# Optimization experiments

Hardware: AMD Instinct MI355X
Metric: run time of the kernel (lower is better)

The kernel has to match this reference:

```python
import jax, jax.numpy as jnp
import numpy as np

B, T, D, H, L, K, DFF = 8, 512, 512, 8, 4, 31, 2048
DK = D // H
PAD = (K - 1) // 2

def _ln(x, g, b, eps=1e-5):
    m = x.mean(-1, keepdims=True)
    v = ((x - m) ** 2).mean(-1, keepdims=True)
    return (x - m) * jax.lax.rsqrt(v + eps) * g + b

def _swish(x):
    return x * jax.nn.sigmoid(x)

def _rel_shift(x):
    # x: [B,H,T,P] with P = 2T-1 (Transformer-XL style shift)
    b, h, q, p = x.shape
    x = jnp.pad(x, ((0, 0), (0, 0), (0, 0), (1, 0)))
    x = x.reshape(b, h, p + 1, q)[:, :, 1:].reshape(b, h, q, p)
    return x

def setup_inputs() -> dict:
    key = jax.random.key(0)
    ks = iter(jax.random.split(key, 64))
    def w(shape, s=0.02):
        return jax.random.normal(next(ks), shape, jnp.float32) * s
    inp = {
        'x': jax.random.normal(next(ks), (B, T, D), jnp.float32),
        'pos_emb': jax.random.normal(next(ks), (1, 2 * T - 1, D), jnp.float32),
        'ln1_g': jnp.ones((L, D)), 'ln1_b': jnp.zeros((L, D)),
        'ff1_w1': w((L, D, DFF)), 'ff1_b1': jnp.zeros((L, DFF)),
        'ff1_w2': w((L, DFF, D)), 'ff1_b2': jnp.zeros((L, D)),
        'lnA_g': jnp.ones((L, D)), 'lnA_b': jnp.zeros((L, D)),
        'Wq': w((L, D, D)), 'bq': jnp.zeros((L, D)),
        'Wk': w((L, D, D)), 'bk': jnp.zeros((L, D)),
        'Wv': w((L, D, D)), 'bv': jnp.zeros((L, D)),
        'Wo': w((L, D, D)), 'bo': jnp.zeros((L, D)),
        'Wpos': w((L, D, D)),
        'pbu': jnp.zeros((L, H, DK)), 'pbv': jnp.zeros((L, H, DK)),
        'lnC_g': jnp.ones((L, D)), 'lnC_b': jnp.zeros((L, D)),
        'pw1_w': w((L, 2 * D, D)), 'pw1_b': jnp.zeros((L, 2 * D)),
        'dw_w': w((L, D, K)), 'dw_b': jnp.zeros((L, D)),
        'cln_g': jnp.ones((L, D)), 'cln_b': jnp.zeros((L, D)),
        'pw2_w': w((L, D, D)), 'pw2_b': jnp.zeros((L, D)),
        'ln2_g': jnp.ones((L, D)), 'ln2_b': jnp.zeros((L, D)),
        'ff2_w1': w((L, D, DFF)), 'ff2_b1': jnp.zeros((L, DFF)),
        'ff2_w2': w((L, DFF, D)), 'ff2_b2': jnp.zeros((L, D)),
        'lnO_g': jnp.ones((L, D)), 'lnO_b': jnp.zeros((L, D)),
    }
    return inp

def reference(x, pos_emb, ln1_g, ln1_b, ff1_w1, ff1_b1, ff1_w2, ff1_b2,
              lnA_g, lnA_b, Wq, bq, Wk, bk, Wv, bv, Wo, bo, Wpos, pbu, pbv,
              lnC_g, lnC_b, pw1_w, pw1_b, dw_w, dw_b, cln_g, cln_b, pw2_w, pw2_b,
              ln2_g, ln2_b, ff2_w1, ff2_b1, ff2_w2, ff2_b2, lnO_g, lnO_b):
    scale = 1.0 / np.sqrt(DK).astype(np.float32)
    for i in range(L):
        # FFN 1 (half-step residual)
        res = x
        y = _ln(x, ln1_g[i], ln1_b[i])
        y = _swish(y @ ff1_w1[i] + ff1_b1[i]) @ ff1_w2[i] + ff1_b2[i]
        res = res + 0.5 * y
        # rel-pos multi-head self-attention
        y = _ln(res, lnA_g[i], lnA_b[i])
        q = (y @ Wq[i] + bq[i]).reshape(B, T, H, DK)
        k = (y @ Wk[i] + bk[i]).reshape(B, T, H, DK)
        v = (y @ Wv[i] + bv[i]).reshape(B, T, H, DK)
        p = (pos_emb @ Wpos[i]).reshape(1, 2 * T - 1, H, DK)
        ac = jnp.einsum('bthd,bshd->bhts', q + pbu[i], k)          # content score
        bd = jnp.einsum('bthd,xshd->bhts', q + pbv[i], p)          # position score
        bd = _rel_shift(bd)[..., :T]
        attn = jax.nn.softmax((ac + bd) * scale, axis=-1)
        o = jnp.einsum('bhts,bshd->bthd', attn, v).reshape(B, T, D)
        res = res + (o @ Wo[i] + bo[i])
        # convolution module
        y = _ln(res, lnC_g[i], lnC_b[i])
        y = y @ pw1_w[i].T + pw1_b[i]                               # (B,T,2D)
        a, g = jnp.split(y, 2, axis=-1)
        y = a * jax.nn.sigmoid(g)                                   # GLU over channels
        y = jax.lax.conv_general_dilated(
            y.transpose(0, 2, 1), dw_w[i][:, None, :],
            window_strides=(1,), padding=[(PAD, PAD)],
            feature_group_count=D,
            dimension_numbers=('NCH', 'OIH', 'NCH'))
        y = y.transpose(0, 2, 1) + dw_b[i]                          # (B,T,D)
        y = _swish(_ln(y, cln_g[i], cln_b[i]))
        y = y @ pw2_w[i].T + pw2_b[i]
        res = res + y
        # FFN 2 (half-step residual)
        y = _ln(res, ln2_g[i], ln2_b[i])
        y = _swish(y @ ff2_w1[i] + ff2_b1[i]) @ ff2_w2[i] + ff2_b2[i]
        res = res + 0.5 * y
        x = _ln(res, lnO_g[i], lnO_b[i])
    return x
```

## Files before the change

kernel.cpp:

```cpp
#include <hip/hip_runtime.h>


typedef unsigned short u16;
typedef unsigned int u32;
typedef __attribute__((ext_vector_type(8))) short bf16x8;
typedef __attribute__((ext_vector_type(4))) float f32x4;

#define DI __device__ __forceinline__

constexpr int CT = 512;
constexpr int CD = 512;
constexpr int CH = 8;
constexpr int CDK = 64;
constexpr int CDFF = 2048;
constexpr int CNBT = 4096;
constexpr int CL = 4;

DI u16 f2bf(float f) {
  u32 u = __builtin_bit_cast(u32, f);
  u = u + 0x7fffu + ((u >> 16) & 1u);
  return (u16)(u >> 16);
}
DI float bf2f(u16 h) { u32 u = ((u32)h) << 16; return __builtin_bit_cast(float, u); }
DI u32 pack2(float a, float b) { return (u32)f2bf(a) | ((u32)f2bf(b) << 16); }
DI float sigm(float x) { return 1.0f / (1.0f + __expf(-x)); }

DI f32x4 MFMA(bf16x8 a, bf16x8 b, f32x4 c) {
  return __builtin_amdgcn_mfma_f32_16x16x32_bf16(a, b, c, 0, 0, 0);
}

DI void gload16(const void* g, void* l) {
  __builtin_amdgcn_global_load_lds((const __attribute__((address_space(1))) void*)g,
                                   (__attribute__((address_space(3))) void*)l, 16, 0, 0);
}

DI float wsum(float v) {
#pragma unroll
  for (int o = 32; o > 0; o >>= 1) v += __shfl_xor(v, o, 64);
  return v;
}

DI void tbody(const float* ip, u16* op, int R, int C, int c0, int r0,
              int tx, int ty) {
  __shared__ float t[32][33];
#pragma unroll
  for (int i = ty; i < 32; i += 8)
    t[i][tx] = ip[(long)(r0 + i) * C + c0 + tx];
  __syncthreads();
#pragma unroll
  for (int i = ty; i < 32; i += 8)
    op[(long)(c0 + i) * R + r0 + tx] = f2bf(t[tx][i]);
}

__global__ __launch_bounds__(256) void tconv2x_k(const float* __restrict__ in0,
                                                 const float* __restrict__ in1,
                                                 u16* __restrict__ out0,
                                                 u16* __restrict__ out1,
                                                 int R, int C) {
  int z = blockIdx.z;
  int l = z & 3;
  const float* ip = (z < 4 ? in0 : in1) + (long)l * R * C;
  u16* op = (z < 4 ? out0 : out1) + (long)l * R * C;
  tbody(ip, op, R, C, blockIdx.x * 32, blockIdx.y * 32, threadIdx.x, threadIdx.y);
}

__global__ __launch_bounds__(256) void tconvQ_k(
    const float* __restrict__ Wq, const float* __restrict__ Wk,
    const float* __restrict__ Wv, const float* __restrict__ Wo,
    const float* __restrict__ Wpos, u16* __restrict__ wt_qkv,
    u16* __restrict__ wt_o, u16* __restrict__ wt_pos) {
  int z = blockIdx.z;
  int sel = z >> 2, l = z & 3;
  const float* ip;
  u16* op;
  const long S = 512L * 512;
  switch (sel) {
    case 0: ip = Wq + l * S; op = wt_qkv + (long)l * 1536 * 512; break;
    case 1: ip = Wk + l * S; op = wt_qkv + (long)l * 1536 * 512 + S; break;
    case 2: ip = Wv + l * S; op = wt_qkv + (long)l * 1536 * 512 + 2 * S; break;
    case 3: ip = Wo + l * S; op = wt_o + l * S; break;
    default: ip = Wpos + l * S; op = wt_pos + l * S; break;
  }
  tbody(ip, op, 512, 512, blockIdx.x * 32, blockIdx.y * 32, threadIdx.x, threadIdx.y);
}

__global__ __launch_bounds__(256) void cvt_k(const float* __restrict__ in,
                                             u16* __restrict__ out, long nIn, long nOut,
                                             long inZ, long outZ) {
  long i = ((long)blockIdx.x * 256 + threadIdx.x) * 4;
  if (i >= nOut) return;
  const float* ip = in + (long)blockIdx.y * inZ;
  u16* op = out + (long)blockIdx.y * outZ;
  u16 o[4];
#pragma unroll
  for (int j = 0; j < 4; ++j) {
    long idx = i + j;
    o[j] = (idx < nIn) ? f2bf(ip[idx]) : (u16)0;
  }
  uint2 st;
  st.x = (u32)o[0] | ((u32)o[1] << 16);
  st.y = (u32)o[2] | ((u32)o[3] << 16);
  *(uint2*)&op[i] = st;
}

__global__ __launch_bounds__(256) void pwperm_k(const float* __restrict__ in,
                                                u16* __restrict__ out) {
  int l = blockIdx.y;
  long i = (long)blockIdx.x * 256 + threadIdx.x;
  long n = i >> 7;
  int c = (int)(i & 127) * 4;
  int q = (int)(n >> 4) & 1;
  long r = (q ? 512 : 0) + ((n >> 5) << 4) + (n & 15);
  const float* ip = in + ((long)l * 1024 + r) * 512 + c;
  float4 v = *(const float4*)ip;
  u16* op = out + ((long)l * 1024 + n) * 512 + c;
  uint2 st;
  st.x = pack2(v.x, v.y);
  st.y = pack2(v.z, v.w);
  *(uint2*)op = st;
}

__global__ __launch_bounds__(256) void dwt_k(const float* __restrict__ in,
                                             float* __restrict__ out) {
  int l = blockIdx.y;
  int idx = blockIdx.x * 256 + threadIdx.x;
  if (idx >= 512 * 31) return;
  int k = idx >> 9, d = idx & 511;
  out[(long)l * 31 * 512 + idx] = in[(long)l * 512 * 31 + d * 31 + k];
}

__global__ __launch_bounds__(256) void qkvbias_k(const float* __restrict__ bq,
                                                 const float* __restrict__ bk,
                                                 const float* __restrict__ bv,
                                                 float* __restrict__ out) {
  int z = blockIdx.y;
  int j = blockIdx.x * 256 + threadIdx.x;
  float v;
  if (j < 512) v = bq[z * 512 + j];
  else if (j < 1024) v = bk[z * 512 + j - 512];
  else v = bv[z * 512 + j - 1024];
  out[z * 1536 + j] = v;
}

__global__ __launch_bounds__(256) void copy_k(const float* __restrict__ in,
                                              float* __restrict__ out) {
  long i = ((long)blockIdx.x * 256 + threadIdx.x) * 4;
  *(float4*)(out + i) = *(const float4*)(in + i);
}

template <int F32OUT>
__global__ __launch_bounds__(256) void ln_k(const float* in, void* out,
                                            const float* gw, const float* bw) {
  int tid = threadIdx.x, wid = tid >> 6, lane = tid & 63;
  long row = (long)blockIdx.x * 4 + wid;
  const float* x = in + row * CD + lane * 8;
  float4 v0 = *(const float4*)x;
  float4 v1 = *(const float4*)(x + 4);
  float s = v0.x + v0.y + v0.z + v0.w + v1.x + v1.y + v1.z + v1.w;
  float q = v0.x * v0.x + v0.y * v0.y + v0.z * v0.z + v0.w * v0.w +
            v1.x * v1.x + v1.y * v1.y + v1.z * v1.z + v1.w * v1.w;
  s = wsum(s);
  q = wsum(q);
  float mean = s * (1.0f / CD);
  float var = q * (1.0f / CD) - mean * mean;
  float rs = rsqrtf(var + 1e-5f);
  int c = lane * 8;
  float4 g0 = *(const float4*)(gw + c), g1 = *(const float4*)(gw + c + 4);
  float4 b0 = *(const float4*)(bw + c), b1 = *(const float4*)(bw + c + 4);
  float y0 = (v0.x - mean) * rs * g0.x + b0.x;
  float y1 = (v0.y - mean) * rs * g0.y + b0.y;
  float y2 = (v0.z - mean) * rs * g0.z + b0.z;
  float y3 = (v0.w - mean) * rs * g0.w + b0.w;
  float y4 = (v1.x - mean) * rs * g1.x + b1.x;
  float y5 = (v1.y - mean) * rs * g1.y + b1.y;
  float y6 = (v1.z - mean) * rs * g1.z + b1.z;
  float y7 = (v1.w - mean) * rs * g1.w + b1.w;
  if (F32OUT) {
    float* o = (float*)out + row * CD + c;
    *(float4*)o = make_float4(y0, y1, y2, y3);
    *(float4*)(o + 4) = make_float4(y4, y5, y6, y7);
  } else {
    u16* o = (u16*)out + row * CD + c;
    uint4 pk;
    pk.x = pack2(y0, y1);
    pk.y = pack2(y2, y3);
    pk.z = pack2(y4, y5);
    pk.w = pack2(y6, y7);
    *(uint4*)o = pk;
  }
}

__global__ __launch_bounds__(256) void lnln_k(float* cur, u16* ybf,
                                              const float* gO, const float* bO,
                                              const float* g1, const float* b1) {
  int tid = threadIdx.x, wid = tid >> 6, lane = tid & 63;
  long row = (long)blockIdx.x * 4 + wid;
  float* x = cur + row * CD + lane * 8;
  float v[8];
  *(float4*)&v[0] = *(const float4*)x;
  *(float4*)&v[4] = *(const float4*)(x + 4);
  float s = 0.f, q = 0.f;
#pragma unroll
  for (int j = 0; j < 8; ++j) { s += v[j]; q += v[j] * v[j]; }
  s = wsum(s);
  q = wsum(q);
  float mean = s * (1.0f / CD);
  float var = q * (1.0f / CD) - mean * mean;
  float rs = rsqrtf(var + 1e-5f);
  int c = lane * 8;
  float y[8];
#pragma unroll
  for (int j = 0; j < 8; ++j) y[j] = (v[j] - mean) * rs * gO[c + j] + bO[c + j];
  *(float4*)x = *(float4*)&y[0];
  *(float4*)(x + 4) = *(float4*)&y[4];
  float s2 = 0.f, q2 = 0.f;
#pragma unroll
  for (int j = 0; j < 8; ++j) { s2 += y[j]; q2 += y[j] * y[j]; }
  s2 = wsum(s2);
  q2 = wsum(q2);
  float mean2 = s2 * (1.0f / CD);
  float var2 = q2 * (1.0f / CD) - mean2 * mean2;
  float rs2 = rsqrtf(var2 + 1e-5f);
  float z[8];
#pragma unroll
  for (int j = 0; j < 8; ++j) z[j] = (y[j] - mean2) * rs2 * g1[c + j] + b1[c + j];
  u16* o = ybf + row * CD + c;
  uint4 pk;
  pk.x = pack2(z[0], z[1]);
  pk.y = pack2(z[2], z[3]);
  pk.z = pack2(z[4], z[5]);
  pk.w = pack2(z[6], z[7]);
  *(uint4*)o = pk;
}

template <int EPI, int SPLITK>
__global__ __launch_bounds__(256, 3) void gemm3_k(
    const u16* __restrict__ A, const u16* __restrict__ B, void* C,
    const float* __restrict__ bias, float alpha, int lda, int ldb, int ldc, int Kd) {
  __shared__ u16 ldsA[2][128 * 64];
  __shared__ u16 ldsB[2][64 * 64];
  const int tid = threadIdx.x, wid = tid >> 6, lane = tid & 63;
  const int m0 = blockIdx.x * 128, n0 = blockIdx.y * 64;
  const int wm = wid >> 1, wn = wid & 1;
  const int fr = lane & 15, fq = lane >> 4;
  const f32x4 vz = {0.f, 0.f, 0.f, 0.f};
  f32x4 acc[4][2] = {{vz, vz}, {vz, vz}, {vz, vz}, {vz, vz}};

  const int Kc = Kd / SPLITK;
  const int kb0 = (SPLITK > 1) ? blockIdx.z * Kc : 0;
  const int nK = Kc / 64;

  auto stage = [&](int buf, int kt) {
    const int k0 = kb0 + kt * 64;
#pragma unroll
    for (int r = 0; r < 4; ++r) {
      int bi = r * 4096 + tid * 16;
      int row = bi >> 7;
      int ch = ((bi >> 4) & 7) ^ (row & 7);
      gload16(A + (long)(m0 + row) * lda + k0 + ch * 8,
              (char*)&ldsA[buf][0] + r * 4096 + wid * 1024);
    }
#pragma unroll
    for (int r = 0; r < 2; ++r) {
      int bi = r * 4096 + tid * 16;
      int row = bi >> 7;
      int ch = ((bi >> 4) & 7) ^ (row & 7);
      gload16(B + (long)(n0 + row) * ldb + k0 + ch * 8,
              (char*)&ldsB[buf][0] + r * 4096 + wid * 1024);
    }
  };

  stage(0, 0);
  asm volatile("s_waitcnt vmcnt(0)" ::: "memory");
  __syncthreads();
  int buf = 0;
  for (int kt = 0; kt < nK; ++kt) {
    if (kt + 1 < nK) stage(buf ^ 1, kt + 1);
#pragma unroll
    for (int ks = 0; ks < 2; ++ks) {
      int ch = ks * 4 + fq;
      bf16x8 af[4], bfv[2];
#pragma unroll
      for (int i = 0; i < 4; ++i) {
        int arow = wm * 64 + i * 16 + fr;
        af[i] = *(const bf16x8*)((const char*)&ldsA[buf][0] + arow * 128 +
                                 ((ch ^ (arow & 7)) << 4));
      }
#pragma unroll
      for (int i = 0; i < 2; ++i) {
        int brow = wn * 32 + i * 16 + fr;
        bfv[i] = *(const bf16x8*)((const char*)&ldsB[buf][0] + brow * 128 +
                                  ((ch ^ (brow & 7)) << 4));
      }
#pragma unroll
      for (int mi = 0; mi < 4; ++mi)
#pragma unroll
        for (int ni = 0; ni < 2; ++ni)
          acc[mi][ni] = MFMA(af[mi], bfv[ni], acc[mi][ni]);
    }
    asm volatile("s_waitcnt vmcnt(0)" ::: "memory");
    __syncthreads();
    buf ^= 1;
  }

  if constexpr (EPI == 7) {
    const int ucol = (n0 >> 1) + wn * 16 + fr;
    float ba = bias[ucol], bg = bias[512 + ucol];
#pragma unroll
    for (int mi = 0; mi < 4; ++mi) {
      const int gmB = m0 + wm * 64 + mi * 16 + fq * 4;
#pragma unroll
      for (int r = 0; r < 4; ++r) {
        float va = acc[mi][0][r] + ba;
        float vg = acc[mi][1][r] + bg;
        ((u16*)C)[(long)(gmB + r) * 512 + ucol] = f2bf(va * sigm(vg));
      }
    }
  } else {
#pragma unroll
    for (int mi = 0; mi < 4; ++mi) {
      const int gmB = m0 + wm * 64 + mi * 16 + fq * 4;
#pragma unroll
      for (int ni = 0; ni < 2; ++ni) {
        const int gn = n0 + wn * 32 + ni * 16 + fr;
        float bv_ = 0.f;
        if constexpr (EPI == 1 || EPI == 2 || EPI == 3) bv_ = bias[gn];
#pragma unroll
        for (int r = 0; r < 4; ++r) {
          const int gm = gmB + r;
          float v = acc[mi][ni][r];
          long idx = (long)gm * ldc + gn;
          if constexpr (EPI == 0) ((u16*)C)[idx] = f2bf(v);
          else if constexpr (EPI == 1) ((u16*)C)[idx] = f2bf(v + bv_);
          else if constexpr (EPI == 2) {
            float x = v + bv_;
            ((u16*)C)[idx] = f2bf(x * sigm(x));
          } else if constexpr (EPI == 3) {
            float* R = (float*)C;
            if constexpr (SPLITK > 1) {
              float add = alpha * (v + (blockIdx.z == 0 ? bv_ : 0.f));
              atomicAdd(&R[idx], add);
            } else {
              R[idx] += alpha * (v + bv_);
            }
          }
        }
      }
    }
  }
}

__global__ __launch_bounds__(256) void vtrans_k(const u16* __restrict__ qkv,
                                                u16* __restrict__ vt) {
  __shared__ u16 t[64][80];
  int tid = threadIdx.x;
  int t0 = blockIdx.x * 64;
  int bh = blockIdx.y, b = bh >> 3, h = bh & 7;
  {
    int tl = tid >> 2, dg = (tid & 3) * 16;
    const u16* src = qkv + ((long)(b * CT + t0 + tl)) * 1536 + 1024 + h * 64 + dg;
    uint4 a0 = *(const uint4*)src;
    uint4 a1 = *(const uint4*)(src + 8);
    *(uint4*)&t[tl][dg] = a0;
    *(uint4*)&t[tl][dg + 8] = a1;
  }
  __syncthreads();
  {
    int dl = tid >> 2, tg = (tid & 3) * 16;
    u16* dst = vt + ((long)bh * 64 + dl) * CT + t0 + tg;
    u16 tmp[16];
#pragma unroll
    for (int j = 0; j < 16; ++j) tmp[j] = t[tg + j][dl];
    uint4 o0, o1;
    o0.x = (u32)tmp[0] | ((u32)tmp[1] << 16);
    o0.y = (u32)tmp[2] | ((u32)tmp[3] << 16);
    o0.z = (u32)tmp[4] | ((u32)tmp[5] << 16);
    o0.w = (u32)tmp[6] | ((u32)tmp[7] << 16);
    o1.x = (u32)tmp[8] | ((u32)tmp[9] << 16);
    o1.y = (u32)tmp[10] | ((u32)tmp[11] << 16);
    o1.z = (u32)tmp[12] | ((u32)tmp[13] << 16);
    o1.w = (u32)tmp[14] | ((u32)tmp[15] << 16);
    *(uint4*)dst = o0;
    *(uint4*)(dst + 8) = o1;
  }
}

__global__ __launch_bounds__(256, 2) void attn_k(
    const u16* __restrict__ qkvp, const u16* __restrict__ pball,
    const float* __restrict__ pbuL, const float* __restrict__ pbvL,
    const u16* __restrict__ vt, u16* __restrict__ out) {
  __shared__ u16 ldsK[2][64 * 64];
  __shared__ u16 ldsP[2][128 * 64];
  __shared__ u16 bd0s[4][16 * 80];
  __shared__ u16 stile[4][16 * 64];
  const int tid = threadIdx.x, wid = tid >> 6, lane = tid & 63;
  const int t0 = blockIdx.x * 64;
  const int bh = blockIdx.y, b = bh >> 3, h = bh & 7;
  const int fr = lane & 15, fq = lane >> 4;

  const u16* kbase = qkvp + (long)(b * CT) * 1536 + 512 + h * 64;
  const u16* pbase = pball + h * 64;
  const float* pu = pbuL + h * 64;
  const float* pv = pbvL + h * 64;

  const u16* qp = qkvp + (long)(b * CT + t0 + wid * 16 + fr) * 1536 + h * 64;
  bf16x8 qua[2], qva[2];
#pragma unroll
  for (int kk = 0; kk < 2; ++kk) {
    bf16x8 qw = *(const bf16x8*)(qp + kk * 32 + fq * 8);
    const float* bu = pu + kk * 32 + fq * 8;
    const float* bv = pv + kk * 32 + fq * 8;
#pragma unroll
    for (int j = 0; j < 8; ++j) {
      float qf = bf2f((u16)qw[j]);
      qua[kk][j] = (short)f2bf(qf + bu[j]);
      qva[kk][j] = (short)f2bf(qf + bv[j]);
    }
  }

  const f32x4 vz = {0.f, 0.f, 0.f, 0.f};
  f32x4 oacc[4] = {vz, vz, vz, vz};
  float m_run[4] = {-1e30f, -1e30f, -1e30f, -1e30f};
  float l_run[4] = {0.f, 0.f, 0.f, 0.f};
  const int jbw = (3 - wid) * 16;

  auto stage = [&](int buf, int st) {
    int s0 = st * 64, j0 = s0 - t0 + 448;
#pragma unroll
    for (int r = 0; r < 2; ++r) {
      int c = r * 256 + tid;
      int row = c >> 3, cs = (c & 7) ^ (row & 7);
      gload16(kbase + (long)(s0 + row) * 1536 + cs * 8,
              (char*)&ldsK[buf][0] + r * 4096 + wid * 1024);
    }
#pragma unroll
    for (int r = 0; r < 4; ++r) {
      int c = r * 256 + tid;
      int row = c >> 3, cs = (c & 7) ^ (row & 7);
      gload16(pbase + (long)(j0 + row) * 2048 + cs * 8,
              (char*)&ldsP[buf][0] + r * 4096 + wid * 1024);
    }
  };

  stage(0, 0);
  int cur = 0;
  for (int st = 0; st < 8; ++st) {
    const int s0 = st * 64;
    if (st + 1 < 8) {
      stage(cur ^ 1, st + 1);
      asm volatile("s_waitcnt vmcnt(6)" ::: "memory");
    } else {
      asm volatile("s_waitcnt vmcnt(0)" ::: "memory");
    }
    __syncthreads();

    bf16x8 vb[4][2];
#pragma unroll
    for (int ni = 0; ni < 4; ++ni)
#pragma unroll
      for (int kk = 0; kk < 2; ++kk)
        vb[ni][kk] = *(const bf16x8*)&vt[((long)bh * 64 + ni * 16 + fr) * 512 +
                                         s0 + kk * 32 + fq * 8];

    f32x4 ac[4] = {vz, vz, vz, vz};
#pragma unroll
    for (int kk = 0; kk < 2; ++kk) {
#pragma unroll
      for (int ni = 0; ni < 4; ++ni) {
        int row = ni * 16 + fr;
        bf16x8 kb = *(const bf16x8*)((const char*)&ldsK[cur][0] +
                                     ((row * 128 + kk * 64 + fq * 16) ^ ((row & 7) << 4)));
        ac[ni] = MFMA(qua[kk], kb, ac[ni]);
      }
    }
    f32x4 bd[5] = {vz, vz, vz, vz, vz};
#pragma unroll
    for (int kk = 0; kk < 2; ++kk) {
#pragma unroll
      for (int nbi = 0; nbi < 5; ++nbi) {
        int row = jbw + nbi * 16 + fr;
        bf16x8 pb = *(const bf16x8*)((const char*)&ldsP[cur][0] +
                                     ((row * 128 + kk * 64 + fq * 16) ^ ((row & 7) << 4)));
        bd[nbi] = MFMA(qva[kk], pb, bd[nbi]);
      }
    }
#pragma unroll
    for (int nbi = 0; nbi < 5; ++nbi)
#pragma unroll
      for (int r = 0; r < 4; ++r)
        bd0s[wid][(fq * 4 + r) * 80 + nbi * 16 + fr] = f2bf(bd[nbi][r]);

    float vals[4][4];
#pragma unroll
    for (int ni = 0; ni < 4; ++ni)
#pragma unroll
      for (int r = 0; r < 4; ++r) {
        int tlw = fq * 4 + r;
        int jcol = ni * 16 + fr + 15 - tlw;
        vals[ni][r] = (ac[ni][r] + bf2f(bd0s[wid][tlw * 80 + jcol])) * 0.125f;
      }
    float scf[4];
#pragma unroll
    for (int r = 0; r < 4; ++r) {
      float mx = fmaxf(fmaxf(vals[0][r], vals[1][r]), fmaxf(vals[2][r], vals[3][r]));
      mx = fmaxf(mx, __shfl_xor(mx, 1));
      mx = fmaxf(mx, __shfl_xor(mx, 2));
      mx = fmaxf(mx, __shfl_xor(mx, 4));
      mx = fmaxf(mx, __shfl_xor(mx, 8));
      float mnew = fmaxf(m_run[r], mx);
      scf[r] = __expf(m_run[r] - mnew);
      m_run[r] = mnew;
      float sum = 0.f;
#pragma unroll
      for (int ni = 0; ni < 4; ++ni) {
        float p = __expf(vals[ni][r] - mnew);
        vals[ni][r] = p;
        sum += p;
      }
      sum += __shfl_xor(sum, 1);
      sum += __shfl_xor(sum, 2);
      sum += __shfl_xor(sum, 4);
      sum += __shfl_xor(sum, 8);
      l_run[r] = l_run[r] * scf[r] + sum;
    }
#pragma unroll
    for (int ni = 0; ni < 4; ++ni)
#pragma unroll
      for (int r = 0; r < 4; ++r) {
        int tlw = fq * 4 + r;
        *(u16*)((char*)&stile[wid][0] +
                (((tlw * 128) + (ni * 16 + fr) * 2) ^ ((tlw & 7) << 4))) =
            f2bf(vals[ni][r]);
      }
#pragma unroll
    for (int ni = 0; ni < 4; ++ni)
#pragma unroll
      for (int r = 0; r < 4; ++r) oacc[ni][r] *= scf[r];
#pragma unroll
    for (int kk = 0; kk < 2; ++kk) {
      bf16x8 pa = *(const bf16x8*)((const char*)&stile[wid][0] +
                                   ((fr * 128 + kk * 64 + fq * 16) ^ ((fr & 7) << 4)));
#pragma unroll
      for (int ni = 0; ni < 4; ++ni) oacc[ni] = MFMA(pa, vb[ni][kk], oacc[ni]);
    }
    __syncthreads();
    cur ^= 1;
  }

  float inv[4];
#pragma unroll
  for (int r = 0; r < 4; ++r) inv[r] = 1.0f / l_run[r];
#pragma unroll
  for (int ni = 0; ni < 4; ++ni)
#pragma unroll
    for (int r = 0; r < 4; ++r) {
      long row = (long)(b * CT + t0 + wid * 16 + fq * 4 + r) * CD + h * CDK;
      out[row + ni * 16 + fr] = f2bf(oacc[ni][r] * inv[r]);
    }
}

__global__ __launch_bounds__(256) void conv2_k(const u16* __restrict__ u,
                                               const float* __restrict__ wT,
                                               const float* __restrict__ wb,
                                               const float* __restrict__ cg,
                                               const float* __restrict__ cb,
                                               u16* __restrict__ out) {
  constexpr int TT = 8;
  int tid = threadIdx.x, d0 = tid * 2;
  int b = blockIdx.y, t0 = blockIdx.x * TT;
  const u16* ub = u + ((long)b * CT) * CD + d0;

  u32 strip[TT + 30];
#pragma unroll
  for (int j = 0; j < TT + 30; ++j) {
    int tt = t0 + j - 15;
    strip[j] = ((unsigned)tt < (unsigned)CT) ? *(const u32*)(ub + (long)tt * CD) : 0u;
  }
  float2 bias = *(const float2*)(wb + d0);
  float a0[TT], a1[TT];
#pragma unroll
  for (int t = 0; t < TT; ++t) { a0[t] = bias.x; a1[t] = bias.y; }
#pragma unroll
  for (int k = 0; k < 31; ++k) {
    float2 wk = *(const float2*)(wT + k * CD + d0);
#pragma unroll
    for (int t = 0; t < TT; ++t) {
      u32 pr = strip[t + k];
      a0[t] += bf2f((u16)(pr & 0xffff)) * wk.x;
      a1[t] += bf2f((u16)(pr >> 16)) * wk.y;
    }
  }
  __shared__ float redS[4][TT], redQ[4][TT];
  int wid = tid >> 6, lane = tid & 63;
#pragma unroll
  for (int t = 0; t < TT; ++t) {
    float s = a0[t] + a1[t];
    float q = a0[t] * a0[t] + a1[t] * a1[t];
    s = wsum(s);
    q = wsum(q);
    if (lane == 0) { redS[wid][t] = s; redQ[wid][t] = q; }
  }
  __syncthreads();
  float2 g2 = *(const float2*)(cg + d0);
  float2 b2 = *(const float2*)(cb + d0);
#pragma unroll
  for (int t = 0; t < TT; ++t) {
    float s = redS[0][t] + redS[1][t] + redS[2][t] + redS[3][t];
    float q = redQ[0][t] + redQ[1][t] + redQ[2][t] + redQ[3][t];
    float mean = s * (1.f / 512), var = q * (1.f / 512) - mean * mean;
    float rs = rsqrtf(var + 1e-5f);
    float y0 = (a0[t] - mean) * rs * g2.x + b2.x;
    float y1 = (a1[t] - mean) * rs * g2.y + b2.y;
    y0 = y0 * sigm(y0);
    y1 = y1 * sigm(y1);
    *(u32*)(out + ((long)(b * CT + t0 + t)) * CD + d0) = pack2(y0, y1);
  }
}

extern "C" void kernel_launch(void* const* d_in, const int* in_sizes, int n_in,
                              void* d_out, int out_size, void* d_ws, size_t ws_size,
                              hipStream_t stream) {
  const float* in_x   = (const float*)d_in[0];
  const float* in_pos = (const float*)d_in[1];
  const float* ln1_g  = (const float*)d_in[2];
  const float* ln1_b  = (const float*)d_in[3];
  const float* ff1_w1 = (const float*)d_in[4];
  const float* ff1_b1 = (const float*)d_in[5];
  const float* ff1_w2 = (const float*)d_in[6];
  const float* ff1_b2 = (const float*)d_in[7];
  const float* lnA_g  = (const float*)d_in[8];
  const float* lnA_b  = (const float*)d_in[9];
  const float* Wq     = (const float*)d_in[10];
  const float* bq     = (const float*)d_in[11];
  const float* Wk     = (const float*)d_in[12];
  const float* bk     = (const float*)d_in[13];
  const float* Wv     = (const float*)d_in[14];
  const float* bv     = (const float*)d_in[15];
  const float* Wo     = (const float*)d_in[16];
  const float* bo     = (const float*)d_in[17];
  const float* Wpos   = (const float*)d_in[18];
  const float* pbu    = (const float*)d_in[19];
  const float* pbv    = (const float*)d_in[20];
  const float* lnC_g  = (const float*)d_in[21];
  const float* lnC_b  = (const float*)d_in[22];
  const float* pw1_w  = (const float*)d_in[23];
  const float* pw1_b  = (const float*)d_in[24];
  const float* dw_w   = (const float*)d_in[25];
  const float* dw_b   = (const float*)d_in[26];
  const float* cln_g  = (const float*)d_in[27];
  const float* cln_b  = (const float*)d_in[28];
  const float* pw2_w  = (const float*)d_in[29];
  const float* pw2_b  = (const float*)d_in[30];
  const float* ln2_g  = (const float*)d_in[31];
  const float* ln2_b  = (const float*)d_in[32];
  const float* ff2_w1 = (const float*)d_in[33];
  const float* ff2_b1 = (const float*)d_in[34];
  const float* ff2_w2 = (const float*)d_in[35];
  const float* ff2_b2 = (const float*)d_in[36];
  const float* lnO_g  = (const float*)d_in[37];
  const float* lnO_b  = (const float*)d_in[38];
  (void)in_sizes; (void)n_in; (void)out_size; (void)ws_size;

  char* ws = (char*)d_ws;
  size_t off = 0;
  auto alloc = [&](size_t bytes) -> void* {
    off = (off + 255) & ~(size_t)255;
    void* p = ws + off;
    off += bytes;
    return p;
  };

  u16* wt_ff1w1 = (u16*)alloc((size_t)CL * CDFF * CD * 2);
  u16* wt_ff1w2 = (u16*)alloc((size_t)CL * CD * CDFF * 2);
  u16* wt_qkv   = (u16*)alloc((size_t)CL * 1536 * CD * 2);
  u16* wt_o     = (u16*)alloc((size_t)CL * CD * CD * 2);
  u16* wt_pos   = (u16*)alloc((size_t)CL * CD * CD * 2);
  u16* w_pw1p   = (u16*)alloc((size_t)CL * 1024 * CD * 2);
  u16* w_pw2    = (u16*)alloc((size_t)CL * CD * CD * 2);
  u16* wt_ff2w1 = (u16*)alloc((size_t)CL * CDFF * CD * 2);
  u16* wt_ff2w2 = (u16*)alloc((size_t)CL * CD * CDFF * 2);
  float* qkvbias = (float*)alloc((size_t)CL * 1536 * 4);
  u16* posbf = (u16*)alloc((size_t)1024 * CD * 2);
  float* dwT = (float*)alloc((size_t)CL * 31 * CD * 4);
  u16* pbf_all = (u16*)alloc((size_t)1024 * 2048 * 2);
  float* cur = (float*)alloc((size_t)CNBT * CD * 4);
  u16* ybf   = (u16*)alloc((size_t)CNBT * CD * 2);
  u16* qkv   = (u16*)alloc((size_t)CNBT * 1536 * 2);
  u16* hbf   = (u16*)alloc((size_t)CNBT * CDFF * 2);
  u16* vt    = (u16*)alloc((size_t)64 * CDK * CT * 2);
  u16* obf   = (u16*)alloc((size_t)CNBT * CD * 2);
  u16* ubuf  = (u16*)alloc((size_t)CNBT * CD * 2);
  u16* cbf   = (u16*)alloc((size_t)CNBT * CD * 2);

  dim3 b256(256);
  dim3 tb(32, 8);

  tconv2x_k<<<dim3(CDFF / 32, CD / 32, 2 * CL), tb, 0, stream>>>(
      ff1_w1, ff2_w1, wt_ff1w1, wt_ff2w1, CD, CDFF);
  tconv2x_k<<<dim3(CD / 32, CDFF / 32, 2 * CL), tb, 0, stream>>>(
      ff1_w2, ff2_w2, wt_ff1w2, wt_ff2w2, CDFF, CD);
  tconvQ_k<<<dim3(CD / 32, CD / 32, 5 * CL), tb, 0, stream>>>(
      Wq, Wk, Wv, Wo, Wpos, wt_qkv, wt_o, wt_pos);
  pwperm_k<<<dim3(512, CL), b256, 0, stream>>>(pw1_w, w_pw1p);
  cvt_k<<<dim3(256, CL, 1), b256, 0, stream>>>(pw2_w, w_pw2, 512L * 512, 512L * 512,
                                               512L * 512, 512L * 512);
  cvt_k<<<dim3(512, 1, 1), b256, 0, stream>>>(in_pos, posbf, 1023L * 512, 1024L * 512, 0, 0);
  dwt_k<<<dim3(62, CL), b256, 0, stream>>>(dw_w, dwT);
  qkvbias_k<<<dim3(6, CL), b256, 0, stream>>>(bq, bk, bv, qkvbias);
  copy_k<<<dim3(2048), b256, 0, stream>>>(in_x, cur);
  gemm3_k<0, 1><<<dim3(8, 32, 1), b256, 0, stream>>>(
      posbf, wt_pos, pbf_all, nullptr, 0.f, CD, CD, 2048, CD);
  ln_k<0><<<dim3(1024), b256, 0, stream>>>(cur, ybf, ln1_g, ln1_b);

  for (int i = 0; i < CL; ++i) {
    const u16* Wf1 = wt_ff1w1 + (long)i * CDFF * CD;
    const u16* Wf2 = wt_ff1w2 + (long)i * CD * CDFF;
    const u16* Wqk = wt_qkv + (long)i * 1536 * CD;
    const u16* Wou = wt_o + (long)i * CD * CD;
    const u16* Wp1 = w_pw1p + (long)i * 1024 * CD;
    const u16* Wp2 = w_pw2 + (long)i * CD * CD;
    const u16* Wf3 = wt_ff2w1 + (long)i * CDFF * CD;
    const u16* Wf4 = wt_ff2w2 + (long)i * CD * CDFF;

    gemm3_k<2, 1><<<dim3(32, 32, 1), b256, 0, stream>>>(
        ybf, Wf1, hbf, ff1_b1 + (long)i * CDFF, 0.f, CD, CD, CDFF, CD);
    gemm3_k<3, 2><<<dim3(32, 8, 2), b256, 0, stream>>>(
        hbf, Wf2, cur, ff1_b2 + i * CD, 0.5f, CDFF, CDFF, CD, CDFF);

    ln_k<0><<<dim3(1024), b256, 0, stream>>>(cur, ybf, lnA_g + i * CD, lnA_b + i * CD);
    gemm3_k<1, 1><<<dim3(32, 24, 1), b256, 0, stream>>>(
        ybf, Wqk, qkv, qkvbias + i * 1536, 0.f, CD, CD, 1536, CD);
    vtrans_k<<<dim3(8, 64), b256, 0, stream>>>(qkv, vt);
    attn_k<<<dim3(8, 64), b256, 0, stream>>>(qkv, pbf_all + i * 512, pbu + i * 512,
                                             pbv + i * 512, vt, obf);
    gemm3_k<3, 2><<<dim3(32, 8, 2), b256, 0, stream>>>(
        obf, Wou, cur, bo + i * CD, 1.0f, CD, CD, CD, CD);

    ln_k<0><<<dim3(1024), b256, 0, stream>>>(cur, ybf, lnC_g + i * CD, lnC_b + i * CD);
    gemm3_k<7, 1><<<dim3(32, 16, 1), b256, 0, stream>>>(
        ybf, Wp1, ubuf, pw1_b + (long)i * 1024, 0.f, CD, CD, 512, CD);
    conv2_k<<<dim3(CT / 8, 8), b256, 0, stream>>>(ubuf, dwT + (long)i * 31 * CD,
                                                  dw_b + i * CD, cln_g + i * CD,
                                                  cln_b + i * CD, cbf);
    gemm3_k<3, 2><<<dim3(32, 8, 2), b256, 0, stream>>>(
        cbf, Wp2, cur, pw2_b + i * CD, 1.0f, CD, CD, CD, CD);

    ln_k<0><<<dim3(1024), b256, 0, stream>>>(cur, ybf, ln2_g + i * CD, ln2_b + i * CD);
    gemm3_k<2, 1><<<dim3(32, 32, 1), b256, 0, stream>>>(
        ybf, Wf3, hbf, ff2_b1 + (long)i * CDFF, 0.f, CD, CD, CDFF, CD);
    gemm3_k<3, 2><<<dim3(32, 8, 2), b256, 0, stream>>>(
        hbf, Wf4, cur, ff2_b2 + i * CD, 0.5f, CDFF, CDFF, CD, CDFF);

    if (i < CL - 1)
      lnln_k<<<dim3(1024), b256, 0, stream>>>(cur, ybf, lnO_g + i * CD, lnO_b + i * CD,
                                              ln1_g + (i + 1) * CD, ln1_b + (i + 1) * CD);
    else
      ln_k<1><<<dim3(1024), b256, 0, stream>>>(cur, d_out, lnO_g + i * CD, lnO_b + i * CD);
  }
}
```

Before: 892.9 us.

## Shrink GEMM tiles to 64x64 and fuse V transpose into QKV epilogue

The GEMM kernel moves from 128x64 to 64x64 output tiles with a shared LDS array, doubling grid sizes to fill more compute units on the 4096-row problems. Both K-substeps of fragments are loaded before the MFMAs are issued. A new epilogue writes the V slice of the QKV projection directly in transposed per-head layout, which removes the separate vtrans kernel launch and its round trip through memory. The Wo and pw2 projections drop split-K atomics in favour of plain accumulation. Smaller tiles lower data reuse per block and raise total global and LDS traffic, and the transposed V stores are narrow 8-byte scattered writes.

Measured after the change: 794.8 us. 11.0% less time.

```diff
diff --git a/kernel.cpp b/kernel.cpp
--- a/kernel.cpp
+++ b/kernel.cpp
@@ -234,17 +234,17 @@
 }
 
 template <int EPI, int SPLITK>
-__global__ __launch_bounds__(256, 3) void gemm3_k(
+__global__ __launch_bounds__(256, 2) void gemm2_k(
     const u16* __restrict__ A, const u16* __restrict__ B, void* C,
+    u16* __restrict__ Caux,
     const float* __restrict__ bias, float alpha, int lda, int ldb, int ldc, int Kd) {
-  __shared__ u16 ldsA[2][128 * 64];
-  __shared__ u16 ldsB[2][64 * 64];
+  __shared__ u16 lds[2][2][64 * 64];
   const int tid = threadIdx.x, wid = tid >> 6, lane = tid & 63;
-  const int m0 = blockIdx.x * 128, n0 = blockIdx.y * 64;
+  const int m0 = blockIdx.x * 64, n0 = blockIdx.y * 64;
   const int wm = wid >> 1, wn = wid & 1;
   const int fr = lane & 15, fq = lane >> 4;
   const f32x4 vz = {0.f, 0.f, 0.f, 0.f};
-  f32x4 acc[4][2] = {{vz, vz}, {vz, vz}, {vz, vz}, {vz, vz}};
+  f32x4 acc[2][2] = {{vz, vz}, {vz, vz}};
 
   const int Kc = Kd / SPLITK;
   const int kb0 = (SPLITK > 1) ? blockIdx.z * Kc : 0;
@@ -253,20 +253,14 @@
   auto stage = [&](int buf, int kt) {
     const int k0 = kb0 + kt * 64;
 #pragma unroll
-    for (int r = 0; r < 4; ++r) {
+    for (int r = 0; r < 2; ++r) {
       int bi = r * 4096 + tid * 16;
       int row = bi >> 7;
       int ch = ((bi >> 4) & 7) ^ (row & 7);
       gload16(A + (long)(m0 + row) * lda + k0 + ch * 8,
-              (char*)&ldsA[buf][0] + r * 4096 + wid * 1024);
-    }
-#pragma unroll
-    for (int r = 0; r < 2; ++r) {
-      int bi = r * 4096 + tid * 16;
-      int row = bi >> 7;
-      int ch = ((bi >> 4) & 7) ^ (row & 7);
+              (char*)&lds[buf][0][0] + r * 4096 + wid * 1024);
       gload16(B + (long)(n0 + row) * ldb + k0 + ch * 8,
-              (char*)&ldsB[buf][0] + r * 4096 + wid * 1024);
+              (char*)&lds[buf][1][0] + r * 4096 + wid * 1024);
     }
   };
 
@@ -276,28 +270,27 @@
   int buf = 0;
   for (int kt = 0; kt < nK; ++kt) {
     if (kt + 1 < nK) stage(buf ^ 1, kt + 1);
+    bf16x8 af[2][2], bfv[2][2];
 #pragma unroll
     for (int ks = 0; ks < 2; ++ks) {
       int ch = ks * 4 + fq;
-      bf16x8 af[4], bfv[2];
-#pragma unroll
-      for (int i = 0; i < 4; ++i) {
-        int arow = wm * 64 + i * 16 + fr;
-        af[i] = *(const bf16x8*)((const char*)&ldsA[buf][0] + arow * 128 +
-                                 ((ch ^ (arow & 7)) << 4));
-      }
 #pragma unroll
       for (int i = 0; i < 2; ++i) {
+        int arow = wm * 32 + i * 16 + fr;
+        af[ks][i] = *(const bf16x8*)((const char*)&lds[buf][0][0] + arow * 128 +
+                                     ((ch ^ (arow & 7)) << 4));
         int brow = wn * 32 + i * 16 + fr;
-        bfv[i] = *(const bf16x8*)((const char*)&ldsB[buf][0] + brow * 128 +
-                                  ((ch ^ (brow & 7)) << 4));
-      }
-#pragma unroll
-      for (int mi = 0; mi < 4; ++mi)
+        bfv[ks][i] = *(const bf16x8*)((const char*)&lds[buf][1][0] + brow * 128 +
+                                      ((ch ^ (brow & 7)) << 4));
+      }
+    }
+#pragma unroll
+    for (int ks = 0; ks < 2; ++ks)
+#pragma unroll
+      for (int mi = 0; mi < 2; ++mi)
 #pragma unroll
         for (int ni = 0; ni < 2; ++ni)
-          acc[mi][ni] = MFMA(af[mi], bfv[ni], acc[mi][ni]);
-    }
+          acc[mi][ni] = MFMA(af[ks][mi], bfv[ks][ni], acc[mi][ni]);
     asm volatile("s_waitcnt vmcnt(0)" ::: "memory");
     __syncthreads();
     buf ^= 1;
@@ -307,8 +300,8 @@
     const int ucol = (n0 >> 1) + wn * 16 + fr;
     float ba = bias[ucol], bg = bias[512 + ucol];
 #pragma unroll
-    for (int mi = 0; mi < 4; ++mi) {
-      const int gmB = m0 + wm * 64 + mi * 16 + fq * 4;
+    for (int mi = 0; mi < 2; ++mi) {
+      const int gmB = m0 + wm * 32 + mi * 16 + fq * 4;
 #pragma unroll
       for (int r = 0; r < 4; ++r) {
         float va = acc[mi][0][r] + ba;
@@ -316,10 +309,41 @@
         ((u16*)C)[(long)(gmB + r) * 512 + ucol] = f2bf(va * sigm(vg));
       }
     }
+  } else if constexpr (EPI == 8) {
+    if (n0 < 1024) {
+#pragma unroll
+      for (int mi = 0; mi < 2; ++mi) {
+        const int gmB = m0 + wm * 32 + mi * 16 + fq * 4;
+#pragma unroll
+        for (int ni = 0; ni < 2; ++ni) {
+          const int gn = n0 + wn * 32 + ni * 16 + fr;
+          float bv_ = bias[gn];
+#pragma unroll
+          for (int r = 0; r < 4; ++r)
+            ((u16*)C)[(long)(gmB + r) * ldc + gn] = f2bf(acc[mi][ni][r] + bv_);
+        }
+      }
+    } else {
+#pragma unroll
+      for (int mi = 0; mi < 2; ++mi) {
+        const int gmB = m0 + wm * 32 + mi * 16 + fq * 4;
+        const int b = gmB >> 9, t = gmB & 511;
+#pragma unroll
+        for (int ni = 0; ni < 2; ++ni) {
+          const int gn = n0 + wn * 32 + ni * 16 + fr;
+          const int h = (gn - 1024) >> 6, d = (gn - 1024) & 63;
+          float bv_ = bias[gn];
+          uint2 pk;
+          pk.x = pack2(acc[mi][ni][0] + bv_, acc[mi][ni][1] + bv_);
+          pk.y = pack2(acc[mi][ni][2] + bv_, acc[mi][ni][3] + bv_);
+          *(uint2*)&Caux[((long)(b * 8 + h) * 64 + d) * 512 + t] = pk;
+        }
+      }
+    }
   } else {
 #pragma unroll
-    for (int mi = 0; mi < 4; ++mi) {
-      const int gmB = m0 + wm * 64 + mi * 16 + fq * 4;
+    for (int mi = 0; mi < 2; ++mi) {
+      const int gmB = m0 + wm * 32 + mi * 16 + fq * 4;
 #pragma unroll
       for (int ni = 0; ni < 2; ++ni) {
         const int gn = n0 + wn * 32 + ni * 16 + fr;
@@ -347,41 +371,6 @@
         }
       }
     }
-  }
-}
-
-__global__ __launch_bounds__(256) void vtrans_k(const u16* __restrict__ qkv,
-                                                u16* __restrict__ vt) {
-  __shared__ u16 t[64][80];
-  int tid = threadIdx.x;
-  int t0 = blockIdx.x * 64;
-  int bh = blockIdx.y, b = bh >> 3, h = bh & 7;
-  {
-    int tl = tid >> 2, dg = (tid & 3) * 16;
-    const u16* src = qkv + ((long)(b * CT + t0 + tl)) * 1536 + 1024 + h * 64 + dg;
-    uint4 a0 = *(const uint4*)src;
-    uint4 a1 = *(const uint4*)(src + 8);
-    *(uint4*)&t[tl][dg] = a0;
-    *(uint4*)&t[tl][dg + 8] = a1;
-  }
-  __syncthreads();
-  {
-    int dl = tid >> 2, tg = (tid & 3) * 16;
-    u16* dst = vt + ((long)bh * 64 + dl) * CT + t0 + tg;
-    u16 tmp[16];
-#pragma unroll
-    for (int j = 0; j < 16; ++j) tmp[j] = t[tg + j][dl];
-    uint4 o0, o1;
-    o0.x = (u32)tmp[0] | ((u32)tmp[1] << 16);
-    o0.y = (u32)tmp[2] | ((u32)tmp[3] << 16);
-    o0.z = (u32)tmp[4] | ((u32)tmp[5] << 16);
-    o0.w = (u32)tmp[6] | ((u32)tmp[7] << 16);
-    o1.x = (u32)tmp[8] | ((u32)tmp[9] << 16);
-    o1.y = (u32)tmp[10] | ((u32)tmp[11] << 16);
-    o1.z = (u32)tmp[12] | ((u32)tmp[13] << 16);
-    o1.w = (u32)tmp[14] | ((u32)tmp[15] << 16);
-    *(uint4*)dst = o0;
-    *(uint4*)(dst + 8) = o1;
   }
 }
 
@@ -708,8 +697,8 @@
   dwt_k<<<dim3(62, CL), b256, 0, stream>>>(dw_w, dwT);
   qkvbias_k<<<dim3(6, CL), b256, 0, stream>>>(bq, bk, bv, qkvbias);
   copy_k<<<dim3(2048), b256, 0, stream>>>(in_x, cur);
-  gemm3_k<0, 1><<<dim3(8, 32, 1), b256, 0, stream>>>(
-      posbf, wt_pos, pbf_all, nullptr, 0.f, CD, CD, 2048, CD);
+  gemm2_k<0, 1><<<dim3(16, 32, 1), b256, 0, stream>>>(
+      posbf, wt_pos, pbf_all, nullptr, nullptr, 0.f, CD, CD, 2048, CD);
   ln_k<0><<<dim3(1024), b256, 0, stream>>>(cur, ybf, ln1_g, ln1_b);
 
   for (int i = 0; i < CL; ++i) {
@@ -722,34 +711,33 @@
     const u16* Wf3 = wt_ff2w1 + (long)i * CDFF * CD;
     const u16* Wf4 = wt_ff2w2 + (long)i * CD * CDFF;
 
-    gemm3_k<2, 1><<<dim3(32, 32, 1), b256, 0, stream>>>(
-        ybf, Wf1, hbf, ff1_b1 + (long)i * CDFF, 0.f, CD, CD, CDFF, CD);
-    gemm3_k<3, 2><<<dim3(32, 8, 2), b256, 0, stream>>>(
-        hbf, Wf2, cur, ff1_b2 + i * CD, 0.5f, CDFF, CDFF, CD, CDFF);
+    gemm2_k<2, 1><<<dim3(64, 32, 1), b256, 0, stream>>>(
+        ybf, Wf1, hbf, nullptr, ff1_b1 + (long)i * CDFF, 0.f, CD, CD, CDFF, CD);
+    gemm2_k<3, 2><<<dim3(64, 8, 2), b256, 0, stream>>>(
+        hbf, Wf2, cur, nullptr, ff1_b2 + i * CD, 0.5f, CDFF, CDFF, CD, CDFF);
 
     ln_k<0><<<dim3(1024), b256, 0, stream>>>(cur, ybf, lnA_g + i * CD, lnA_b + i * CD);
-    gemm3_k<1, 1><<<dim3(32, 24, 1), b256, 0, stream>>>(
-        ybf, Wqk, qkv, qkvbias + i * 1536, 0.f, CD, CD, 1536, CD);
-    vtrans_k<<<dim3(8, 64), b256, 0, stream>>>(qkv, vt);
+    gemm2_k<8, 1><<<dim3(64, 24, 1), b256, 0, stream>>>(
+        ybf, Wqk, qkv, vt, qkvbias + i * 1536, 0.f, CD, CD, 1536, CD);
     attn_k<<<dim3(8, 64), b256, 0, stream>>>(qkv, pbf_all + i * 512, pbu + i * 512,
                                              pbv + i * 512, vt, obf);
-    gemm3_k<3, 2><<<dim3(32, 8, 2), b256, 0, stream>>>(
-        obf, Wou, cur, bo + i * CD, 1.0f, CD, CD, CD, CD);
+    gemm2_k<3, 1><<<dim3(64, 8, 1), b256, 0, stream>>>(
+        obf, Wou, cur, nullptr, bo + i * CD, 1.0f, CD, CD, CD, CD);
 
     ln_k<0><<<dim3(1024), b256, 0, stream>>>(cur, ybf, lnC_g + i * CD, lnC_b + i * CD);
-    gemm3_k<7, 1><<<dim3(32, 16, 1), b256, 0, stream>>>(
-        ybf, Wp1, ubuf, pw1_b + (long)i * 1024, 0.f, CD, CD, 512, CD);
+    gemm2_k<7, 1><<<dim3(64, 16, 1), b256, 0, stream>>>(
+        ybf, Wp1, ubuf, nullptr, pw1_b + (long)i * 1024, 0.f, CD, CD, 512, CD);
     conv2_k<<<dim3(CT / 8, 8), b256, 0, stream>>>(ubuf, dwT + (long)i * 31 * CD,
                                                   dw_b + i * CD, cln_g + i * CD,
                                                   cln_b + i * CD, cbf);
-    gemm3_k<3, 2><<<dim3(32, 8, 2), b256, 0, stream>>>(
-        cbf, Wp2, cur, pw2_b + i * CD, 1.0f, CD, CD, CD, CD);
+    gemm2_k<3, 1><<<dim3(64, 8, 1), b256, 0, stream>>>(
+        cbf, Wp2, cur, nullptr, pw2_b + i * CD, 1.0f, CD, CD, CD, CD);
 
     ln_k<0><<<dim3(1024), b256, 0, stream>>>(cur, ybf, ln2_g + i * CD, ln2_b + i * CD);
-    gemm3_k<2, 1><<<dim3(32, 32, 1), b256, 0, stream>>>(
-        ybf, Wf3, hbf, ff2_b1 + (long)i * CDFF, 0.f, CD, CD, CDFF, CD);
-    gemm3_k<3, 2><<<dim3(32, 8, 2), b256, 0, stream>>>(
-        hbf, Wf4, cur, ff2_b2 + i * CD, 0.5f, CDFF, CDFF, CD, CDFF);
+    gemm2_k<2, 1><<<dim3(64, 32, 1), b256, 0, stream>>>(
+        ybf, Wf3, hbf, nullptr, ff2_b1 + (long)i * CDFF, 0.f, CD, CD, CDFF, CD);
+    gemm2_k<3, 2><<<dim3(64, 8, 2), b256, 0, stream>>>(
+        hbf, Wf4, cur, nullptr, ff2_b2 + i * CD, 0.5f, CDFF, CDFF, CD, CDFF);
 
     if (i < CL - 1)
       lnln_k<<<dim3(1024), b256, 0, stream>>>(cur, ybf, lnO_g + i * CD, lnO_b + i * CD,
```
